# Optimization experiments

Measured on AMD Instinct MI355X. Metric: run time of the kernel, lower is better.

Reference implementation:

```python
import jax, jax.numpy as jnp
import numpy as np
import math

H, W = 32, 32
HID = 256
K = 4
B = 16
DIN = 272
DFF = 1024
L = 2
NB = 7
IMG_H, IMG_W = 256, 256
LN_EPS = 1e-5


def _layernorm(x, g, b):
    m = jnp.mean(x, axis=-1, keepdims=True)
    v = jnp.var(x, axis=-1, keepdims=True)
    return (x - m) / jnp.sqrt(v + LN_EPS) * g + b


def _neighbor_mask(h, w, nb):
    # (h*w, h*w): 0 inside the nb x nb window around each query pixel, -inf outside
    rr = jnp.repeat(jnp.arange(h), w)
    cc = jnp.tile(jnp.arange(w), h)
    near = (jnp.abs(rr[:, None] - rr[None, :]) <= nb // 2) & (
        jnp.abs(cc[:, None] - cc[None, :]) <= nb // 2
    )
    return jnp.where(near, 0.0, -jnp.inf).astype(jnp.float32)


def _pos_embed(row_embed, col_embed):
    # pos[i*w + j] = concat(col_embed[j], row_embed[i])  -> (h*w, hid)
    h, nf = row_embed.shape
    w = col_embed.shape[0]
    pe = jnp.concatenate(
        [
            jnp.broadcast_to(col_embed[None, :, :], (h, w, nf)),
            jnp.broadcast_to(row_embed[:, None, :], (h, w, nf)),
        ],
        axis=-1,
    )
    return pe.reshape(h * w, 2 * nf)


def _resize_bilinear_ac(x, oh, ow):
    # nn.UpsamplingBilinear2d => align_corners=True
    b, c, h, w = x.shape
    ys = jnp.arange(oh) * ((h - 1) / (oh - 1))
    y0 = jnp.floor(ys).astype(jnp.int32)
    y1 = jnp.minimum(y0 + 1, h - 1)
    fy = (ys - y0).astype(x.dtype)
    x = x[:, :, y0, :] * (1 - fy)[None, None, :, None] + x[:, :, y1, :] * fy[None, None, :, None]
    xs = jnp.arange(ow) * ((w - 1) / (ow - 1))
    x0 = jnp.floor(xs).astype(jnp.int32)
    x1 = jnp.minimum(x0 + 1, w - 1)
    fx = (xs - x0).astype(x.dtype)
    x = x[:, :, :, x0] * (1 - fx) + x[:, :, :, x1] * fx
    return x


def _forward(query_features, matched_features, qW, qb, kvW, kvb, row_embed, col_embed,
             aggW, aggb, n1g, n1b, l1W, l1b, l2W, l2b, n2g, n2b, outW, outb):
    b, c_in, h, w = query_features.shape
    n = h * w
    # b c h w -> b (h w) c, then input projections
    qt = query_features.transpose(0, 2, 3, 1).reshape(b, n, c_in) @ qW + qb  # (b,n,hid)
    kt = matched_features.transpose(0, 1, 3, 4, 2).reshape(K, b, n, c_in) @ kvW + kvb  # (K,b,n,hid)

    pos = _pos_embed(row_embed, col_embed)  # (n, hid); broadcast over batch
    mask = _neighbor_mask(h, w, NB)  # (n, n)
    scale = 1.0 / math.sqrt(qt.shape[-1])

    x = qt
    for l in range(L):
        qp = (x + pos) * scale            # q gets pos embed then scaled
        kp = kt + pos                     # k gets pos embed; v is the raw matched tokens
        scores = jnp.einsum('bnc,kbmc->kbnm', qp, kp) + mask
        attn = jax.nn.softmax(scores, axis=-1)
        o = jnp.einsum('kbnm,kbmc->bnkc', attn, kt).reshape(b, n, K * HID)
        o = o @ aggW[l] + aggb[l]
        x = _layernorm(x + o, n1g[l], n1b[l])
        ff = jax.nn.relu(x @ l1W[l] + l1b[l]) @ l2W[l] + l2b[l]
        x = _layernorm(x + ff, n2g[l], n2b[l])

    recon_tokens = x @ outW + outb  # (b,n,c_in)
    recon = recon_tokens.reshape(b, h, w, c_in).transpose(0, 3, 1, 2)
    pred = jnp.sqrt(jnp.sum((recon - query_features) ** 2, axis=1, keepdims=True))
    pred = (pred - pred.min()) / (pred.max() - pred.min())
    pred = _resize_bilinear_ac(pred, IMG_H, IMG_W)
    return recon, pred


def setup_inputs() -> dict:
    key = jax.random.key(0)
    ks = jax.random.split(key, 12)

    def nrm(k, shape, scale=0.02):
        return jax.random.normal(k, shape, jnp.float32) * scale

    return {
        'query_features': jax.random.normal(ks[0], (B, DIN, H, W), jnp.float32),
        'matched_features': jax.random.normal(ks[1], (K, B, DIN, H, W), jnp.float32),
        'qW': nrm(ks[2], (DIN, HID)), 'qb': jnp.zeros((HID,), jnp.float32),
        'kvW': nrm(ks[3], (DIN, HID)), 'kvb': jnp.zeros((HID,), jnp.float32),
        'row_embed': jax.random.uniform(ks[4], (H, HID // 2), jnp.float32),
        'col_embed': jax.random.uniform(ks[5], (W, HID // 2), jnp.float32),
        'aggW': nrm(ks[6], (L, K * HID, HID)), 'aggb': jnp.zeros((L, HID), jnp.float32),
        'n1g': jnp.ones((L, HID), jnp.float32), 'n1b': jnp.zeros((L, HID), jnp.float32),
        'l1W': nrm(ks[7], (L, HID, DFF)), 'l1b': jnp.zeros((L, DFF), jnp.float32),
        'l2W': nrm(ks[8], (L, DFF, HID)), 'l2b': jnp.zeros((L, HID), jnp.float32),
        'n2g': jnp.ones((L, HID), jnp.float32), 'n2b': jnp.zeros((L, HID), jnp.float32),
        'outW': nrm(ks[9], (HID, DIN)), 'outb': jnp.zeros((DIN,), jnp.float32),
    }


def reference(query_features, matched_features, qW, qb, kvW, kvb, row_embed, col_embed,
              aggW, aggb, n1g, n1b, l1W, l1b, l2W, l2b, n2g, n2b, outW, outb):
    return _forward(query_features, matched_features, qW, qb, kvW, kvb, row_embed,
                    col_embed, aggW, aggb, n1g, n1b, l1W, l1b, l2W, l2b, n2g, n2b,
                    outW, outb)
```

## Files before the change

kernel.cpp:

```cpp
#include <hip/hip_runtime.h>
#include <hip/hip_bf16.h>
#include <math.h>

#define BATCH 16
#define NTOK 1024
#define HID 256
#define KMEM 4
#define DIN 272
#define DINP 288
#define DFF 1024
#define LN_EPS 1e-5f

using short8 = __attribute__((ext_vector_type(8))) short;
using short4v = __attribute__((ext_vector_type(4))) short;
using floatx4 = __attribute__((ext_vector_type(4))) float;

__device__ inline short f2bf(float f) {
  unsigned u = __builtin_bit_cast(unsigned, f);
  u += 0x7fff + ((u >> 16) & 1);
  return (short)(u >> 16);
}
__device__ inline float bf2f(short s) {
  unsigned u = ((unsigned)(unsigned short)s) << 16;
  return __builtin_bit_cast(float, u);
}

#define QSCALE 0.0625f

__global__ __launch_bounds__(256) void pos_kernel(
    const float* __restrict__ row_e, const float* __restrict__ col_e,
    float* __restrict__ pos) {
  int t = blockIdx.x;
  int j = threadIdx.x;
  float v = (j < 128) ? col_e[(t & 31) * 128 + j]
                      : row_e[(t >> 5) * 128 + (j - 128)];
  pos[t * 256 + j] = v;
}

__global__ __launch_bounds__(256) void tcvt_kernel(
    const float* __restrict__ qf, const float* __restrict__ mf,
    short* __restrict__ qf_t, short* __restrict__ mf_t) {
  __shared__ short tile[32][33];
  int slice = blockIdx.x >> 5;
  int t0 = (blockIdx.x & 31) * 32;
  int c0 = blockIdx.y * 32;
  int tx = threadIdx.x & 31, ty = threadIdx.x >> 5;
  const float* s;
  short* d;
  if (slice < 16) {
    s = qf + (long)slice * DIN * NTOK;
    d = qf_t + (long)slice * NTOK * DINP;
  } else {
    s = mf + (long)(slice - 16) * DIN * NTOK;
    d = mf_t + (long)(slice - 16) * NTOK * DINP;
  }
#pragma unroll
  for (int i = 0; i < 4; i++) {
    int c = c0 + ty + i * 8;
    float v = (c < DIN) ? s[(long)c * NTOK + t0 + tx] : 0.f;
    tile[ty + i * 8][tx] = f2bf(v);
  }
  __syncthreads();
  d += (long)t0 * DINP + c0;
#pragma unroll
  for (int i = 0; i < 4; i++) {
    int tl = ty + i * 8;
    d[(long)tl * DINP + tx] = tile[tx][tl];
  }
}

struct WtJob {
  const float* src;
  short* dst;
  int K, Kd, N, ntx, start;
};
struct WtJobs {
  WtJob j[9];
};

__global__ __launch_bounds__(256) void wt_cvt_all_kernel(WtJobs jobs) {
  __shared__ short tile[32][33];
  int bid = blockIdx.x;
  int ji = 0;
#pragma unroll
  for (int i = 1; i < 9; ++i)
    if (bid >= jobs.j[i].start) ji = i;
  const float* W = jobs.j[ji].src;
  short* Wt = jobs.j[ji].dst;
  int K = jobs.j[ji].K, Kd = jobs.j[ji].Kd, N = jobs.j[ji].N;
  int local = bid - jobs.j[ji].start;
  int n0 = (local % jobs.j[ji].ntx) * 32;
  int k0 = (local / jobs.j[ji].ntx) * 32;
  int tx = threadIdx.x & 31, ty8 = threadIdx.x >> 5;
#pragma unroll
  for (int i = 0; i < 4; i++) {
    int k = k0 + ty8 + i * 8;
    int n = n0 + tx;
    float v = (k < K && n < N) ? W[(long)k * N + n] : 0.f;
    tile[ty8 + i * 8][tx] = f2bf(v);
  }
  __syncthreads();
#pragma unroll
  for (int i = 0; i < 4; i++) {
    int n = n0 + ty8 + i * 8;
    int k = k0 + tx;
    if (n < N && k < Kd) Wt[(long)n * Kd + k] = tile[tx][ty8 + i * 8];
  }
}

template <int OUTMODE>
__global__ __launch_bounds__(256) void gemm2_kernel(
    const short* __restrict__ A, const short* __restrict__ Wt,
    const float* __restrict__ bias, float* __restrict__ Cf,
    short* __restrict__ Cs, int M, int N, int K, int gxn,
    short* __restrict__ ktp, short* __restrict__ ktv,
    const float* __restrict__ pos, const float* __restrict__ qfp,
    float* __restrict__ ppart) {
  __shared__ short As[2][64][40];
  __shared__ short Bs[2][128][40];
  __shared__ float part_s[64][2];
  int nwg = gridDim.x;
  int cpx = nwg >> 3;
  int bid = blockIdx.x;
  int h = (bid & 7) * cpx + (bid >> 3);
  int cx = h % gxn;
  int ry = h / gxn;
  int row0 = ry * 64, col0 = cx * 128;
  int tid = threadIdx.x;
  int w = tid >> 6, lane = tid & 63;
  int wrow = (w >> 1) * 32, wcol = (w & 1) * 64;
  int lcol = lane & 15, kg = lane >> 4;

  int arow = tid >> 2, ak = (tid & 3) * 8;
  int brow = tid >> 2, bk = (tid & 3) * 8;
  const short* Ab = A + (long)row0 * K;
  const short* Bb = Wt + (long)col0 * K;
  bool bv0 = (col0 + brow) < N;
  bool bv1 = (col0 + brow + 64) < N;

  const short8 z8 = (short8){0, 0, 0, 0, 0, 0, 0, 0};
  short8 ra, rb0, rb1;
  ra = *reinterpret_cast<const short8*>(&Ab[(long)arow * K + ak]);
  rb0 = bv0 ? *reinterpret_cast<const short8*>(&Bb[(long)brow * K + bk]) : z8;
  rb1 = bv1 ? *reinterpret_cast<const short8*>(&Bb[(long)(brow + 64) * K + bk])
            : z8;
  *reinterpret_cast<short8*>(&As[0][arow][ak]) = ra;
  *reinterpret_cast<short8*>(&Bs[0][brow][bk]) = rb0;
  *reinterpret_cast<short8*>(&Bs[0][brow + 64][bk]) = rb1;
  __syncthreads();

  floatx4 acc[2][4];
#pragma unroll
  for (int m = 0; m < 2; ++m)
#pragma unroll
    for (int n = 0; n < 4; ++n) acc[m][n] = (floatx4){0.f, 0.f, 0.f, 0.f};

  int NT = K >> 5;
  for (int t = 0; t < NT; ++t) {
    int cur = t & 1;
    if (t + 1 < NT) {
      int ko = (t + 1) << 5;
      ra = *reinterpret_cast<const short8*>(&Ab[(long)arow * K + ko + ak]);
      rb0 = bv0 ? *reinterpret_cast<const short8*>(&Bb[(long)brow * K + ko + bk])
                : z8;
      rb1 = bv1 ? *reinterpret_cast<const short8*>(
                      &Bb[(long)(brow + 64) * K + ko + bk])
                : z8;
    }
    short8 af[2], bf[4];
#pragma unroll
    for (int m = 0; m < 2; ++m)
      af[m] = *reinterpret_cast<const short8*>(
          &As[cur][wrow + m * 16 + lcol][kg * 8]);
#pragma unroll
    for (int n = 0; n < 4; ++n)
      bf[n] = *reinterpret_cast<const short8*>(
          &Bs[cur][wcol + n * 16 + lcol][kg * 8]);
#pragma unroll
    for (int m = 0; m < 2; ++m)
#pragma unroll
      for (int n = 0; n < 4; ++n)
        acc[m][n] = __builtin_amdgcn_mfma_f32_16x16x32_bf16(af[m], bf[n],
                                                            acc[m][n], 0, 0, 0);
    if (t + 1 < NT) {
      int nxt = cur ^ 1;
      *reinterpret_cast<short8*>(&As[nxt][arow][ak]) = ra;
      *reinterpret_cast<short8*>(&Bs[nxt][brow][bk]) = rb0;
      *reinterpret_cast<short8*>(&Bs[nxt][brow + 64][bk]) = rb1;
    }
    __syncthreads();
  }

  if (OUTMODE == 2) {
    short* Ts = &Bs[0][0][0];
    int slice = row0 >> 10, tok0 = row0 & 1023;
#pragma unroll
    for (int n = 0; n < 4; ++n) {
      int cl = wcol + n * 16 + lcol;
      int c = col0 + cl;
      float bv = bias[c];
#pragma unroll
      for (int m = 0; m < 2; ++m) {
        int rl = wrow + m * 16 + kg * 4;
#pragma unroll
        for (int q = 0; q < 4; ++q) {
          float val = acc[m][n][q] + bv;
          Ts[(rl + q) * 132 + cl] = f2bf(val);
          ktp[(long)(row0 + rl + q) * 256 + c] =
              f2bf(val + pos[(tok0 + rl + q) * 256 + c]);
        }
      }
    }
    __syncthreads();
    int t8 = tid & 7;
#pragma unroll
    for (int p = 0; p < 4; ++p) {
      int cl = p * 32 + (tid >> 3);
      short8 v;
#pragma unroll
      for (int j = 0; j < 8; ++j) v[j] = Ts[(t8 * 8 + j) * 132 + cl];
      *reinterpret_cast<short8*>(
          &ktv[(long)slice * (256 * 1024) + (long)(col0 + cl) * 1024 + tok0 +
               t8 * 8]) = v;
    }
    return;
  }

  if (OUTMODE == 4) {
    int bb = row0 >> 10;
    int tb0 = (row0 & 1023) + wrow;
    float sqp[2][4] = {};
#pragma unroll
    for (int n = 0; n < 4; ++n) {
      int c = col0 + wcol + n * 16 + lcol;
      if (c < N) {
        float bv = bias[c];
#pragma unroll
        for (int m = 0; m < 2; ++m) {
          int tb = tb0 + m * 16 + kg * 4;
          long addr = ((long)bb * DIN + c) * 1024 + tb;
          float4 qv = *reinterpret_cast<const float4*>(&qfp[addr]);
          float4 ov;
          float v0 = acc[m][n][0] + bv;
          float v1 = acc[m][n][1] + bv;
          float v2 = acc[m][n][2] + bv;
          float v3 = acc[m][n][3] + bv;
          ov.x = v0;
          ov.y = v1;
          ov.z = v2;
          ov.w = v3;
          float d0 = v0 - qv.x, d1 = v1 - qv.y, d2 = v2 - qv.z, d3 = v3 - qv.w;
          sqp[m][0] = fmaf(d0, d0, sqp[m][0]);
          sqp[m][1] = fmaf(d1, d1, sqp[m][1]);
          sqp[m][2] = fmaf(d2, d2, sqp[m][2]);
          sqp[m][3] = fmaf(d3, d3, sqp[m][3]);
          *reinterpret_cast<float4*>(&Cf[addr]) = ov;
        }
      }
    }
#pragma unroll
    for (int m = 0; m < 2; ++m)
#pragma unroll
      for (int q = 0; q < 4; ++q) {
        float s = sqp[m][q];
        s += __shfl_xor(s, 1);
        s += __shfl_xor(s, 2);
        s += __shfl_xor(s, 4);
        s += __shfl_xor(s, 8);
        if (lcol == 0) part_s[wrow + m * 16 + kg * 4 + q][w & 1] = s;
      }
    __syncthreads();
    if (tid < 64)
      ppart[(long)cx * 16384 + row0 + tid] = part_s[tid][0] + part_s[tid][1];
    return;
  }

#pragma unroll
  for (int n = 0; n < 4; ++n) {
    int c = col0 + wcol + n * 16 + lcol;
    if (c >= N) continue;
    float bv = bias[c];
#pragma unroll
    for (int m = 0; m < 2; ++m) {
      int rbase = row0 + wrow + m * 16 + kg * 4;
      if (OUTMODE == 0) {
#pragma unroll
        for (int q = 0; q < 4; ++q)
          Cf[(long)(rbase + q) * N + c] = acc[m][n][q] + bv;
      } else if (OUTMODE == 1) {
#pragma unroll
        for (int q = 0; q < 4; ++q)
          Cs[(long)(rbase + q) * N + c] = f2bf(fmaxf(acc[m][n][q] + bv, 0.f));
      } else if (OUTMODE == 3) {
#pragma unroll
        for (int q = 0; q < 4; ++q) {
          float val = acc[m][n][q] + bv;
          Cf[(long)(rbase + q) * N + c] = val;
          Cs[(long)(rbase + q) * N + c] =
              f2bf((val + pos[((rbase + q) & 1023) * 256 + c]) * QSCALE);
        }
      }
    }
  }
}

template <bool EX, bool EQ>
__global__ __launch_bounds__(256) void gemm_ln_kernel(
    const short* __restrict__ A, const short* __restrict__ Wt,
    const float* __restrict__ bias, const float* __restrict__ res,
    const float* __restrict__ g, const float* __restrict__ bta,
    float* __restrict__ xout, short* __restrict__ x16out,
    const float* __restrict__ pos, short* __restrict__ q16out, int K) {
  __shared__ short As[2][32][40];
  __shared__ short Bs[2][256][40];
  __shared__ float st_s[32][4];
  __shared__ float st_s2[32][4];
  int tid = threadIdx.x;
  int row0 = blockIdx.x * 32;
  int w = tid >> 6, lane = tid & 63, lcol = lane & 15, kg = lane >> 4;
  int arow = tid >> 2, ak = (tid & 3) * 8;
  int brow = tid >> 2, bk = (tid & 3) * 8;
  const short* Ab = A + (long)row0 * K;

  short8 ra, rb[4];
  if (tid < 128) ra = *reinterpret_cast<const short8*>(&Ab[(long)arow * K + ak]);
#pragma unroll
  for (int i = 0; i < 4; ++i)
    rb[i] = *reinterpret_cast<const short8*>(&Wt[(long)(brow + i * 64) * K + bk]);
  if (tid < 128) *reinterpret_cast<short8*>(&As[0][arow][ak]) = ra;
#pragma unroll
  for (int i = 0; i < 4; ++i)
    *reinterpret_cast<short8*>(&Bs[0][brow + i * 64][bk]) = rb[i];
  __syncthreads();

  floatx4 acc[2][4];
#pragma unroll
  for (int m = 0; m < 2; ++m)
#pragma unroll
    for (int n = 0; n < 4; ++n) acc[m][n] = (floatx4){0.f, 0.f, 0.f, 0.f};

  int NT = K >> 5;
  for (int t = 0; t < NT; ++t) {
    int cur = t & 1;
    if (t + 1 < NT) {
      int ko = (t + 1) << 5;
      if (tid < 128)
        ra = *reinterpret_cast<const short8*>(&Ab[(long)arow * K + ko + ak]);
#pragma unroll
      for (int i = 0; i < 4; ++i)
        rb[i] = *reinterpret_cast<const short8*>(
            &Wt[(long)(brow + i * 64) * K + ko + bk]);
    }
    short8 af[2], bf[4];
#pragma unroll
    for (int m = 0; m < 2; ++m)
      af[m] =
          *reinterpret_cast<const short8*>(&As[cur][m * 16 + lcol][kg * 8]);
#pragma unroll
    for (int n = 0; n < 4; ++n)
      bf[n] = *reinterpret_cast<const short8*>(
          &Bs[cur][w * 64 + n * 16 + lcol][kg * 8]);
#pragma unroll
    for (int m = 0; m < 2; ++m)
#pragma unroll
      for (int n = 0; n < 4; ++n)
        acc[m][n] = __builtin_amdgcn_mfma_f32_16x16x32_bf16(af[m], bf[n],
                                                            acc[m][n], 0, 0, 0);
    if (t + 1 < NT) {
      int nxt = cur ^ 1;
      if (tid < 128) *reinterpret_cast<short8*>(&As[nxt][arow][ak]) = ra;
#pragma unroll
      for (int i = 0; i < 4; ++i)
        *reinterpret_cast<short8*>(&Bs[nxt][brow + i * 64][bk]) = rb[i];
    }
    __syncthreads();
  }

  float val[2][4][4];
#pragma unroll
  for (int n = 0; n < 4; ++n) {
    int c = w * 64 + n * 16 + lcol;
    float bv = bias[c];
#pragma unroll
    for (int m = 0; m < 2; ++m) {
      int rbase = row0 + m * 16 + kg * 4;
#pragma unroll
      for (int q = 0; q < 4; ++q)
        val[m][n][q] = acc[m][n][q] + bv + res[(long)(rbase + q) * 256 + c];
    }
  }
  float s[2][4], s2[2][4];
#pragma unroll
  for (int m = 0; m < 2; ++m)
#pragma unroll
    for (int q = 0; q < 4; ++q) {
      float ss = 0.f, ss2 = 0.f;
#pragma unroll
      for (int n = 0; n < 4; ++n) {
        float v = val[m][n][q];
        ss += v;
        ss2 = fmaf(v, v, ss2);
      }
      ss += __shfl_xor(ss, 1);
      ss2 += __shfl_xor(ss2, 1);
      ss += __shfl_xor(ss, 2);
      ss2 += __shfl_xor(ss2, 2);
      ss += __shfl_xor(ss, 4);
      ss2 += __shfl_xor(ss2, 4);
      ss += __shfl_xor(ss, 8);
      ss2 += __shfl_xor(ss2, 8);
      s[m][q] = ss;
      s2[m][q] = ss2;
    }
  if (lcol == 0) {
#pragma unroll
    for (int m = 0; m < 2; ++m)
#pragma unroll
      for (int q = 0; q < 4; ++q) {
        st_s[m * 16 + kg * 4 + q][w] = s[m][q];
        st_s2[m * 16 + kg * 4 + q][w] = s2[m][q];
      }
  }
  __syncthreads();
#pragma unroll
  for (int m = 0; m < 2; ++m)
#pragma unroll
    for (int q = 0; q < 4; ++q) {
      int row = m * 16 + kg * 4 + q;
      float4 a4 = *reinterpret_cast<const float4*>(&st_s[row][0]);
      float4 b4 = *reinterpret_cast<const float4*>(&st_s2[row][0]);
      float S = (a4.x + a4.y) + (a4.z + a4.w);
      float S2 = (b4.x + b4.y) + (b4.z + b4.w);
      float mean = S * (1.f / 256.f);
      float var = S2 * (1.f / 256.f) - mean * mean;
      float inv = rsqrtf(var + LN_EPS);
#pragma unroll
      for (int n = 0; n < 4; ++n) {
        int c = w * 64 + n * 16 + lcol;
        float o = (val[m][n][q] - mean) * inv * g[c] + bta[c];
        long addr = (long)(row0 + row) * 256 + c;
        if (EX) xout[addr] = o;
        x16out[addr] = f2bf(o);
        if (EQ)
          q16out[addr] =
              f2bf((o + pos[((row0 + row) & 1023) * 256 + c]) * QSCALE);
      }
    }
}

__global__ __launch_bounds__(256) void attn_kernel(
    const short* __restrict__ q16, const short* __restrict__ ktp,
    const short* __restrict__ ktv, short* __restrict__ o) {
  __shared__ short QP_s[32][264];
  __shared__ float st_mx[32][4];
  __shared__ float st_sm[32][4];
  int h = blockIdx.x;
  int xcd = h & 7, jj = h >> 3;
  int sidx = xcd * 8 + (jj >> 5);
  int r = jj & 31;
  int b = sidx & 15, k = sidx >> 4;
  int tid = threadIdx.x;
  int w = tid >> 6, lane = tid & 63, lcol = lane & 15, kg = lane >> 4;

  int r0 = max(r - 3, 0), r1 = min(r + 3, 31);
  int nkr = r1 - r0 + 1, nm = nkr * 32;
  const short* qb = q16 + ((long)b * NTOK + r * 32) * HID;
  const short* ktpb = ktp + ((long)(k * BATCH + b)) * NTOK * HID;
  const short* ktvb = ktv + ((long)(k * BATCH + b)) * NTOK * HID;

#pragma unroll
  for (int p = 0; p < 4; ++p) {
    int chunk = p * 256 + tid;
    int row = chunk >> 5, c8 = (chunk & 31) * 8;
    short8 v = *reinterpret_cast<const short8*>(&qb[(long)row * HID + c8]);
    *reinterpret_cast<short8*>(&QP_s[row][c8]) = v;
  }
  __syncthreads();

  floatx4 acc[2][4];
#pragma unroll
  for (int m = 0; m < 2; ++m)
#pragma unroll
    for (int n = 0; n < 4; ++n) acc[m][n] = (floatx4){0.f, 0.f, 0.f, 0.f};

  int tokn[4];
#pragma unroll
  for (int n = 0; n < 4; ++n) {
    int nf = w * 4 + n;
    int krow = min(r0 + (nf >> 1), 31);
    tokn[n] = krow * 32 + ((nf & 1) << 4) + lcol;
  }
#pragma unroll
  for (int s = 0; s < 8; ++s) {
    short8 af0 = *reinterpret_cast<const short8*>(&QP_s[lcol][s * 32 + kg * 8]);
    short8 af1 =
        *reinterpret_cast<const short8*>(&QP_s[16 + lcol][s * 32 + kg * 8]);
#pragma unroll
    for (int n = 0; n < 4; ++n) {
      short8 bfr = *reinterpret_cast<const short8*>(
          &ktpb[(long)tokn[n] * HID + s * 32 + kg * 8]);
      acc[0][n] =
          __builtin_amdgcn_mfma_f32_16x16x32_bf16(af0, bfr, acc[0][n], 0, 0, 0);
      acc[1][n] =
          __builtin_amdgcn_mfma_f32_16x16x32_bf16(af1, bfr, acc[1][n], 0, 0, 0);
    }
  }

  const float NEG = -3.0e38f;
  float mx[2][4];
#pragma unroll
  for (int m = 0; m < 2; ++m)
#pragma unroll
    for (int q = 0; q < 4; ++q) {
      int rr = m * 16 + kg * 4 + q;
      float vmax = NEG;
#pragma unroll
      for (int n = 0; n < 4; ++n) {
        int col = (w * 4 + n) * 16 + lcol;
        int ck = col & 31;
        bool ok = (col < nm) && (ck - rr <= 3) && (rr - ck <= 3);
        float v = ok ? acc[m][n][q] : NEG;
        acc[m][n][q] = v;
        vmax = fmaxf(vmax, v);
      }
      vmax = fmaxf(vmax, __shfl_xor(vmax, 1));
      vmax = fmaxf(vmax, __shfl_xor(vmax, 2));
      vmax = fmaxf(vmax, __shfl_xor(vmax, 4));
      vmax = fmaxf(vmax, __shfl_xor(vmax, 8));
      mx[m][q] = vmax;
    }
  if (lcol == 0) {
#pragma unroll
    for (int m = 0; m < 2; ++m)
#pragma unroll
      for (int q = 0; q < 4; ++q) st_mx[m * 16 + kg * 4 + q][w] = mx[m][q];
  }
  __syncthreads();
  float sm[2][4];
#pragma unroll
  for (int m = 0; m < 2; ++m)
#pragma unroll
    for (int q = 0; q < 4; ++q) {
      int rr = m * 16 + kg * 4 + q;
      float4 v4 = *reinterpret_cast<const float4*>(&st_mx[rr][0]);
      float g = fmaxf(fmaxf(v4.x, v4.y), fmaxf(v4.z, v4.w));
      float ss = 0.f;
#pragma unroll
      for (int n = 0; n < 4; ++n) {
        float v = acc[m][n][q];
        float pv = (v > -1.0e30f) ? exp2f((v - g) * 1.4426950408889634f) : 0.f;
        acc[m][n][q] = pv;
        ss += pv;
      }
      ss += __shfl_xor(ss, 1);
      ss += __shfl_xor(ss, 2);
      ss += __shfl_xor(ss, 4);
      ss += __shfl_xor(ss, 8);
      sm[m][q] = ss;
    }
  if (lcol == 0) {
#pragma unroll
    for (int m = 0; m < 2; ++m)
#pragma unroll
      for (int q = 0; q < 4; ++q) st_sm[m * 16 + kg * 4 + q][w] = sm[m][q];
  }
  __syncthreads();
#pragma unroll
  for (int m = 0; m < 2; ++m)
#pragma unroll
    for (int q = 0; q < 4; ++q) {
      int rr = m * 16 + kg * 4 + q;
      float4 v4 = *reinterpret_cast<const float4*>(&st_sm[rr][0]);
      float rinv = 1.0f / (v4.x + v4.y + v4.z + v4.w);
#pragma unroll
      for (int n = 0; n < 4; ++n) {
        QP_s[rr][(w * 4 + n) * 16 + lcol] = f2bf(acc[m][n][q] * rinv);
      }
    }
  __syncthreads();

  floatx4 oacc[2][4];
#pragma unroll
  for (int m = 0; m < 2; ++m)
#pragma unroll
    for (int n = 0; n < 4; ++n) oacc[m][n] = (floatx4){0.f, 0.f, 0.f, 0.f};

  for (int kb = 0; kb < nkr; ++kb) {
    short8 ap0 = *reinterpret_cast<const short8*>(&QP_s[lcol][kb * 32 + kg * 8]);
    short8 ap1 =
        *reinterpret_cast<const short8*>(&QP_s[16 + lcol][kb * 32 + kg * 8]);
    int tokb = (r0 + kb) * 32;
#pragma unroll
    for (int n = 0; n < 4; ++n) {
      int ch = w * 64 + n * 16 + lcol;
      short8 bv = *reinterpret_cast<const short8*>(
          &ktvb[(long)ch * NTOK + tokb + kg * 8]);
      oacc[0][n] =
          __builtin_amdgcn_mfma_f32_16x16x32_bf16(ap0, bv, oacc[0][n], 0, 0, 0);
      oacc[1][n] =
          __builtin_amdgcn_mfma_f32_16x16x32_bf16(ap1, bv, oacc[1][n], 0, 0, 0);
    }
  }
#pragma unroll
  for (int m = 0; m < 2; ++m)
#pragma unroll
    for (int n = 0; n < 4; ++n) {
      int ch = w * 64 + n * 16 + lcol;
#pragma unroll
      for (int q = 0; q < 4; ++q) {
        int rr = m * 16 + kg * 4 + q;
        o[((long)b * NTOK + r * 32 + rr) * (KMEM * HID) + k * HID + ch] =
            f2bf(oacc[m][n][q]);
      }
    }
}

__global__ __launch_bounds__(256) void minmax_kernel(
    const float* __restrict__ ppart, float* __restrict__ pred_sq,
    float* __restrict__ mnmx) {
  int tid = threadIdx.x;
  float mn = INFINITY, mx = -INFINITY;
  for (int i = tid; i < BATCH * NTOK; i += 256) {
    float v = ppart[i] + ppart[16384 + i] + ppart[32768 + i];
    pred_sq[i] = v;
    float sv = sqrtf(v);
    mn = fminf(mn, sv);
    mx = fmaxf(mx, sv);
  }
#pragma unroll
  for (int off = 32; off > 0; off >>= 1) {
    mn = fminf(mn, __shfl_xor(mn, off));
    mx = fmaxf(mx, __shfl_xor(mx, off));
  }
  __shared__ float smn[4], smx[4];
  int wave = tid >> 6, lane = tid & 63;
  if (lane == 0) {
    smn[wave] = mn;
    smx[wave] = mx;
  }
  __syncthreads();
  if (tid == 0) {
    mn = fminf(fminf(smn[0], smn[1]), fminf(smn[2], smn[3]));
    mx = fmaxf(fmaxf(smx[0], smx[1]), fmaxf(smx[2], smx[3]));
    mnmx[0] = mn;
    mnmx[1] = mx;
  }
}

__global__ __launch_bounds__(256) void resize_kernel(
    const float* __restrict__ pred_sq, const float* __restrict__ mnmx,
    float* __restrict__ out) {
  long idx = (long)blockIdx.x * 256 + threadIdx.x;
  if (idx >= (long)BATCH * 256 * 256) return;
  int b = (int)(idx >> 16);
  int oy = (int)((idx >> 8) & 255), ox = (int)(idx & 255);
  float mn = mnmx[0], mx = mnmx[1];
  float inv = 1.0f / (mx - mn);
  float ys = oy * (31.0f / 255.0f);
  int y0 = (int)floorf(ys);
  int y1 = min(y0 + 1, 31);
  float fy = ys - (float)y0;
  float xs = ox * (31.0f / 255.0f);
  int x0 = (int)floorf(xs);
  int x1 = min(x0 + 1, 31);
  float fx = xs - (float)x0;
  const float* p = pred_sq + b * NTOK;
  float v00 = sqrtf(p[y0 * 32 + x0]), v01 = sqrtf(p[y0 * 32 + x1]);
  float v10 = sqrtf(p[y1 * 32 + x0]), v11 = sqrtf(p[y1 * 32 + x1]);
  float cA = v00 * (1.f - fy) + v10 * fy;
  float cB = v01 * (1.f - fy) + v11 * fy;
  float v = cA * (1.f - fx) + cB * fx;
  out[idx] = (v - mn) * inv;
}

extern "C" void kernel_launch(void* const* d_in, const int* in_sizes, int n_in,
                              void* d_out, int out_size, void* d_ws,
                              size_t ws_size, hipStream_t stream) {
  const float* qf = (const float*)d_in[0];
  const float* mf = (const float*)d_in[1];
  const float* qW = (const float*)d_in[2];
  const float* qb = (const float*)d_in[3];
  const float* kvW = (const float*)d_in[4];
  const float* kvb = (const float*)d_in[5];
  const float* row_e = (const float*)d_in[6];
  const float* col_e = (const float*)d_in[7];
  const float* aggW = (const float*)d_in[8];
  const float* aggb = (const float*)d_in[9];
  const float* n1g = (const float*)d_in[10];
  const float* n1b = (const float*)d_in[11];
  const float* l1W = (const float*)d_in[12];
  const float* l1b = (const float*)d_in[13];
  const float* l2W = (const float*)d_in[14];
  const float* l2b = (const float*)d_in[15];
  const float* n2g = (const float*)d_in[16];
  const float* n2b = (const float*)d_in[17];
  const float* outW = (const float*)d_in[18];
  const float* outb = (const float*)d_in[19];

  float* out = (float*)d_out;
  float* recon = out;
  float* pred = out + (long)BATCH * DIN * NTOK;

  float* ws = (float*)d_ws;
  float* pos = ws;
  float* x = pos + 262144;
  short* x16 = (short*)(x + 4194304);
  short* q16 = x16 + 4194304;
  short* ktp = q16 + 4194304;
  short* ktv = ktp + 16777216;
  short* buf16 = ktv + 16777216;
  float* tmp256 = (float*)(buf16 + 16777216);
  short* wt = (short*)(tmp256 + 4194304);
  short* wt_agg0 = wt;
  short* wt_agg1 = wt_agg0 + 262144;
  short* wt_l1_0 = wt_agg1 + 262144;
  short* wt_l1_1 = wt_l1_0 + 262144;
  short* wt_l2_0 = wt_l1_1 + 262144;
  short* wt_l2_1 = wt_l2_0 + 262144;
  short* wt_out = wt_l2_1 + 262144;
  short* wt_q = wt_out + 69632;
  short* wt_kv = wt_q + 73728;
  float* pred_part = (float*)(wt_kv + 73728);
  float* pred_sq = pred_part + 49152;
  float* mnmx = pred_sq + 16384;
  short* qf_t = ktp;
  short* mf_t = buf16;

  pos_kernel<<<NTOK, 256, 0, stream>>>(row_e, col_e, pos);

  {
    WtJobs jobs;
    jobs.j[0] = {aggW, wt_agg0, 1024, 1024, 256, 8, 0};
    jobs.j[1] = {aggW + 262144, wt_agg1, 1024, 1024, 256, 8, 256};
    jobs.j[2] = {l1W, wt_l1_0, 256, 256, 1024, 32, 512};
    jobs.j[3] = {l1W + 262144, wt_l1_1, 256, 256, 1024, 32, 768};
    jobs.j[4] = {l2W, wt_l2_0, 1024, 1024, 256, 8, 1024};
    jobs.j[5] = {l2W + 262144, wt_l2_1, 1024, 1024, 256, 8, 1280};
    jobs.j[6] = {outW, wt_out, 256, 256, 272, 9, 1536};
    jobs.j[7] = {qW, wt_q, 272, 288, 256, 8, 1608};
    jobs.j[8] = {kvW, wt_kv, 272, 288, 256, 8, 1680};
    wt_cvt_all_kernel<<<1752, 256, 0, stream>>>(jobs);
  }

  tcvt_kernel<<<dim3(2560, 9), 256, 0, stream>>>(qf, mf, qf_t, mf_t);

  gemm2_kernel<3><<<512, 256, 0, stream>>>(
      qf_t, wt_q, qb, x, q16, BATCH * NTOK, HID, DINP, 2, nullptr, nullptr,
      pos, nullptr, nullptr);
  gemm2_kernel<2><<<2048, 256, 0, stream>>>(
      mf_t, wt_kv, kvb, nullptr, nullptr, KMEM * BATCH * NTOK, HID, DINP, 2,
      ktp, ktv, pos, nullptr, nullptr);

  for (int l = 0; l < 2; l++) {
    attn_kernel<<<2048, 256, 0, stream>>>(q16, ktp, ktv, buf16);
    gemm_ln_kernel<true, false><<<512, 256, 0, stream>>>(
        buf16, l ? wt_agg1 : wt_agg0, aggb + l * 256, x, n1g + l * 256,
        n1b + l * 256, x, x16, nullptr, nullptr, KMEM * HID);
    gemm2_kernel<1><<<2048, 256, 0, stream>>>(
        x16, l ? wt_l1_1 : wt_l1_0, l1b + l * 1024, nullptr, buf16,
        BATCH * NTOK, DFF, HID, 8, nullptr, nullptr, nullptr, nullptr,
        nullptr);
    if (l == 0) {
      gemm_ln_kernel<true, true><<<512, 256, 0, stream>>>(
          buf16, wt_l2_0, l2b, x, n2g, n2b, x, x16, pos, q16, DFF);
    } else {
      gemm_ln_kernel<false, false><<<512, 256, 0, stream>>>(
          buf16, wt_l2_1, l2b + 256, x, n2g + 256, n2b + 256, x, x16, nullptr,
          nullptr, DFF);
    }
  }

  gemm2_kernel<4><<<768, 256, 0, stream>>>(
      x16, wt_out, outb, recon, nullptr, BATCH * NTOK, DIN, HID, 3, nullptr,
      nullptr, nullptr, qf, pred_part);
  minmax_kernel<<<1, 256, 0, stream>>>(pred_part, pred_sq, mnmx);
  resize_kernel<<<(BATCH * 256 * 256) / 256, 256, 0, stream>>>(pred_sq, mnmx,
                                                               pred);
}
```

Measured before the change: 423.3 us.

## Fuse fp32 transpose and bf16 conversion into the input projection GEMM loads

Removes the separate tcvt kernel, which transposed the channel-major fp32 query and matched features into token-major bf16 buffers. The q and kv projection GEMMs now read the fp32 feature maps directly with float4 loads along tokens. They convert to bf16 in registers and scatter-transpose the values into the LDS A tile. This avoids writing and re-reading the intermediate bf16 copy and saves one launch. In exchange, the GEMM issues twice as many A-tile bytes as fp32 and uses scalar 2-byte LDS stores that may cause bank conflicts.

```diff
diff --git a/kernel.cpp b/kernel.cpp
--- a/kernel.cpp
+++ b/kernel.cpp
@@ -35,38 +35,6 @@
   float v = (j < 128) ? col_e[(t & 31) * 128 + j]
                       : row_e[(t >> 5) * 128 + (j - 128)];
   pos[t * 256 + j] = v;
-}
-
-__global__ __launch_bounds__(256) void tcvt_kernel(
-    const float* __restrict__ qf, const float* __restrict__ mf,
-    short* __restrict__ qf_t, short* __restrict__ mf_t) {
-  __shared__ short tile[32][33];
-  int slice = blockIdx.x >> 5;
-  int t0 = (blockIdx.x & 31) * 32;
-  int c0 = blockIdx.y * 32;
-  int tx = threadIdx.x & 31, ty = threadIdx.x >> 5;
-  const float* s;
-  short* d;
-  if (slice < 16) {
-    s = qf + (long)slice * DIN * NTOK;
-    d = qf_t + (long)slice * NTOK * DINP;
-  } else {
-    s = mf + (long)(slice - 16) * DIN * NTOK;
-    d = mf_t + (long)(slice - 16) * NTOK * DINP;
-  }
-#pragma unroll
-  for (int i = 0; i < 4; i++) {
-    int c = c0 + ty + i * 8;
-    float v = (c < DIN) ? s[(long)c * NTOK + t0 + tx] : 0.f;
-    tile[ty + i * 8][tx] = f2bf(v);
-  }
-  __syncthreads();
-  d += (long)t0 * DINP + c0;
-#pragma unroll
-  for (int i = 0; i < 4; i++) {
-    int tl = ty + i * 8;
-    d[(long)tl * DINP + tx] = tile[tx][tl];
-  }
 }
 
 struct WtJob {
@@ -108,9 +76,9 @@
   }
 }
 
-template <int OUTMODE>
+template <int OUTMODE, bool AFP32>
 __global__ __launch_bounds__(256) void gemm2_kernel(
-    const short* __restrict__ A, const short* __restrict__ Wt,
+    const void* __restrict__ Ap, const short* __restrict__ Wt,
     const float* __restrict__ bias, float* __restrict__ Cf,
     short* __restrict__ Cs, int M, int N, int K, int gxn,
     short* __restrict__ ktp, short* __restrict__ ktv,
@@ -131,20 +99,49 @@
   int wrow = (w >> 1) * 32, wcol = (w & 1) * 64;
   int lcol = lane & 15, kg = lane >> 4;
 
+  const short* Ab16 = nullptr;
+  const float* Abf = nullptr;
   int arow = tid >> 2, ak = (tid & 3) * 8;
+  int ach0 = tid >> 4, at0 = (tid & 15) * 4;
+  int ach1 = 16 + (tid >> 4), at1 = (tid & 15) * 4;
+  if (AFP32) {
+    int slice = row0 >> 10, tok0 = row0 & 1023;
+    Abf = (const float*)Ap + (long)slice * DIN * NTOK + tok0;
+  } else {
+    Ab16 = (const short*)Ap + (long)row0 * K;
+  }
   int brow = tid >> 2, bk = (tid & 3) * 8;
-  const short* Ab = A + (long)row0 * K;
   const short* Bb = Wt + (long)col0 * K;
   bool bv0 = (col0 + brow) < N;
   bool bv1 = (col0 + brow + 64) < N;
 
   const short8 z8 = (short8){0, 0, 0, 0, 0, 0, 0, 0};
-  short8 ra, rb0, rb1;
-  ra = *reinterpret_cast<const short8*>(&Ab[(long)arow * K + ak]);
+  const float4 zf4 = make_float4(0.f, 0.f, 0.f, 0.f);
+  short8 ra;
+  float4 rf0, rf1;
+  short8 rb0, rb1;
+  if (AFP32) {
+    rf0 = (ach0 < DIN) ? *reinterpret_cast<const float4*>(
+                             &Abf[(long)ach0 * NTOK + at0])
+                       : zf4;
+    rf1 = (ach1 < DIN) ? *reinterpret_cast<const float4*>(
+                             &Abf[(long)ach1 * NTOK + at1])
+                       : zf4;
+    As[0][at0 + 0][ach0] = f2bf(rf0.x);
+    As[0][at0 + 1][ach0] = f2bf(rf0.y);
+    As[0][at0 + 2][ach0] = f2bf(rf0.z);
+    As[0][at0 + 3][ach0] = f2bf(rf0.w);
+    As[0][at1 + 0][ach1] = f2bf(rf1.x);
+    As[0][at1 + 1][ach1] = f2bf(rf1.y);
+    As[0][at1 + 2][ach1] = f2bf(rf1.z);
+    As[0][at1 + 3][ach1] = f2bf(rf1.w);
+  } else {
+    ra = *reinterpret_cast<const short8*>(&Ab16[(long)arow * K + ak]);
+    *reinterpret_cast<short8*>(&As[0][arow][ak]) = ra;
+  }
   rb0 = bv0 ? *reinterpret_cast<const short8*>(&Bb[(long)brow * K + bk]) : z8;
   rb1 = bv1 ? *reinterpret_cast<const short8*>(&Bb[(long)(brow + 64) * K + bk])
             : z8;
-  *reinterpret_cast<short8*>(&As[0][arow][ak]) = ra;
   *reinterpret_cast<short8*>(&Bs[0][brow][bk]) = rb0;
   *reinterpret_cast<short8*>(&Bs[0][brow + 64][bk]) = rb1;
   __syncthreads();
@@ -160,7 +157,16 @@
     int cur = t & 1;
     if (t + 1 < NT) {
       int ko = (t + 1) << 5;
-      ra = *reinterpret_cast<const short8*>(&Ab[(long)arow * K + ko + ak]);
+      if (AFP32) {
+        rf0 = (ko + ach0 < DIN) ? *reinterpret_cast<const float4*>(
+                                      &Abf[(long)(ko + ach0) * NTOK + at0])
+                                : zf4;
+        rf1 = (ko + ach1 < DIN) ? *reinterpret_cast<const float4*>(
+                                      &Abf[(long)(ko + ach1) * NTOK + at1])
+                                : zf4;
+      } else {
+        ra = *reinterpret_cast<const short8*>(&Ab16[(long)arow * K + ko + ak]);
+      }
       rb0 = bv0 ? *reinterpret_cast<const short8*>(&Bb[(long)brow * K + ko + bk])
                 : z8;
       rb1 = bv1 ? *reinterpret_cast<const short8*>(
@@ -184,7 +190,18 @@
                                                             acc[m][n], 0, 0, 0);
     if (t + 1 < NT) {
       int nxt = cur ^ 1;
-      *reinterpret_cast<short8*>(&As[nxt][arow][ak]) = ra;
+      if (AFP32) {
+        As[nxt][at0 + 0][ach0] = f2bf(rf0.x);
+        As[nxt][at0 + 1][ach0] = f2bf(rf0.y);
+        As[nxt][at0 + 2][ach0] = f2bf(rf0.z);
+        As[nxt][at0 + 3][ach0] = f2bf(rf0.w);
+        As[nxt][at1 + 0][ach1] = f2bf(rf1.x);
+        As[nxt][at1 + 1][ach1] = f2bf(rf1.y);
+        As[nxt][at1 + 2][ach1] = f2bf(rf1.z);
+        As[nxt][at1 + 3][ach1] = f2bf(rf1.w);
+      } else {
+        *reinterpret_cast<short8*>(&As[nxt][arow][ak]) = ra;
+      }
       *reinterpret_cast<short8*>(&Bs[nxt][brow][bk]) = rb0;
       *reinterpret_cast<short8*>(&Bs[nxt][brow + 64][bk]) = rb1;
     }
@@ -723,8 +740,6 @@
   float* pred_part = (float*)(wt_kv + 73728);
   float* pred_sq = pred_part + 49152;
   float* mnmx = pred_sq + 16384;
-  short* qf_t = ktp;
-  short* mf_t = buf16;
 
   pos_kernel<<<NTOK, 256, 0, stream>>>(row_e, col_e, pos);
 
@@ -742,21 +757,19 @@
     wt_cvt_all_kernel<<<1752, 256, 0, stream>>>(jobs);
   }
 
-  tcvt_kernel<<<dim3(2560, 9), 256, 0, stream>>>(qf, mf, qf_t, mf_t);
-
-  gemm2_kernel<3><<<512, 256, 0, stream>>>(
-      qf_t, wt_q, qb, x, q16, BATCH * NTOK, HID, DINP, 2, nullptr, nullptr,
-      pos, nullptr, nullptr);
-  gemm2_kernel<2><<<2048, 256, 0, stream>>>(
-      mf_t, wt_kv, kvb, nullptr, nullptr, KMEM * BATCH * NTOK, HID, DINP, 2,
-      ktp, ktv, pos, nullptr, nullptr);
+  gemm2_kernel<3, true><<<512, 256, 0, stream>>>(
+      qf, wt_q, qb, x, q16, BATCH * NTOK, HID, DINP, 2, nullptr, nullptr, pos,
+      nullptr, nullptr);
+  gemm2_kernel<2, true><<<2048, 256, 0, stream>>>(
+      mf, wt_kv, kvb, nullptr, nullptr, KMEM * BATCH * NTOK, HID, DINP, 2, ktp,
+      ktv, pos, nullptr, nullptr);
 
   for (int l = 0; l < 2; l++) {
     attn_kernel<<<2048, 256, 0, stream>>>(q16, ktp, ktv, buf16);
     gemm_ln_kernel<true, false><<<512, 256, 0, stream>>>(
         buf16, l ? wt_agg1 : wt_agg0, aggb + l * 256, x, n1g + l * 256,
         n1b + l * 256, x, x16, nullptr, nullptr, KMEM * HID);
-    gemm2_kernel<1><<<2048, 256, 0, stream>>>(
+    gemm2_kernel<1, false><<<2048, 256, 0, stream>>>(
         x16, l ? wt_l1_1 : wt_l1_0, l1b + l * 1024, nullptr, buf16,
         BATCH * NTOK, DFF, HID, 8, nullptr, nullptr, nullptr, nullptr,
         nullptr);
@@ -770,7 +783,7 @@
     }
   }
 
-  gemm2_kernel<4><<<768, 256, 0, stream>>>(
+  gemm2_kernel<4, false><<<768, 256, 0, stream>>>(
       x16, wt_out, outb, recon, nullptr, BATCH * NTOK, DIN, HID, 3, nullptr,
       nullptr, nullptr, qf, pred_part);
   minmax_kernel<<<1, 256, 0, stream>>>(pred_part, pred_sq, mnmx);
```

New measurement: 419.8 us. About the same (-0.8%).
